# Performance work log

Measured on AMD Instinct MI355X. Metric: run time of the kernel, lower is better.

The kernel has to match this reference:

```python
import jax, jax.numpy as jnp
import numpy as np

N_STEPS = 5
N_ETYPES = 4
N_GRAPHS = 64
HEADS = 2
N, E, D = 50000, 600000, 128
C = 32


def setup_inputs() -> dict:
    key = jax.random.key(0)
    ks = jax.random.split(key, 24)
    s = 0.08  # param scale to keep activations well-conditioned
    return {
        "in_feat1": jax.random.normal(ks[0], (N, D), jnp.float32),
        "in_feat2": jax.random.normal(ks[1], (N, D), jnp.float32),
        "src1": jax.random.randint(ks[2], (E,), 0, N, jnp.int32),
        "dst1": jax.random.randint(ks[3], (E,), 0, N, jnp.int32),
        "etype1": jax.random.randint(ks[4], (E,), 0, N_ETYPES, jnp.int32),
        "gid1": jnp.sort(jax.random.randint(ks[5], (N,), 0, N_GRAPHS, jnp.int32)),
        "src2": jax.random.randint(ks[6], (E,), 0, N, jnp.int32),
        "dst2": jax.random.randint(ks[7], (E,), 0, N, jnp.int32),
        "etype2": jax.random.randint(ks[8], (E,), 0, N_ETYPES, jnp.int32),
        "gid2": jnp.sort(jax.random.randint(ks[9], (N,), 0, N_GRAPHS, jnp.int32)),
        "W_et": jax.random.normal(ks[10], (N_ETYPES, D, D), jnp.float32) * s,
        "b_et": jax.random.normal(ks[11], (N_ETYPES, D), jnp.float32) * s,
        "W_ih": jax.random.normal(ks[12], (3 * D, D), jnp.float32) * s,
        "W_hh": jax.random.normal(ks[13], (3 * D, D), jnp.float32) * s,
        "b_ih": jax.random.normal(ks[14], (3 * D,), jnp.float32) * s,
        "b_hh": jax.random.normal(ks[15], (3 * D,), jnp.float32) * s,
        "W_fc": jax.random.normal(ks[16], (HEADS * D, D), jnp.float32) * s,
        "attn_l": jax.random.normal(ks[17], (HEADS, D), jnp.float32) * s,
        "attn_r": jax.random.normal(ks[18], (HEADS, D), jnp.float32) * s,
        "gat_bias": jax.random.normal(ks[19], (HEADS * D,), jnp.float32) * s,
        "W_cls": jax.random.normal(ks[20], (C, D), jnp.float32) * s,
        "b_cls": jax.random.normal(ks[21], (C,), jnp.float32) * s,
    }


def _ggann(feat, src, dst, etype, gid,
           W_et, b_et, W_ih, W_hh, b_ih, b_hh,
           W_fc, attn_l, attn_r, gat_bias, W_cls, b_cls):
    n = feat.shape[0]
    h = feat  # in_feats == out_feats -> no zero-padding needed
    # ---- GatedGraphConv: n_steps of per-etype message passing + GRU ----
    for _ in range(N_STEPS):
        # per-etype linear on all nodes: [K, N, D]
        t = jnp.einsum('kod,nd->kno', W_et, h) + b_et[:, None, :]
        msg = t[etype, src]                         # [E, D] gather by (etype, src)
        a = jax.ops.segment_sum(msg, dst, num_segments=n)  # [N, D]
        # GRUCell(a, h)
        gi = a @ W_ih.T + b_ih                      # [N, 3D]
        gh = h @ W_hh.T + b_hh
        i_r, i_z, i_n = jnp.split(gi, 3, axis=1)
        h_r, h_z, h_n = jnp.split(gh, 3, axis=1)
        r = jax.nn.sigmoid(i_r + h_r)
        z = jax.nn.sigmoid(i_z + h_z)
        nn_ = jnp.tanh(i_n + r * h_n)
        h = (1.0 - z) * nn_ + z * h
    # F.normalize (L2 over dim=1) then sigmoid
    h = h / jnp.maximum(jnp.linalg.norm(h, axis=1, keepdims=True), 1e-12)
    h = jax.nn.sigmoid(h)
    # ---- GATConv (num_heads=2) ----
    zft = (h @ W_fc.T).reshape(n, HEADS, D)         # [N, H, D]
    el = jnp.sum(zft * attn_l[None], axis=-1)       # [N, H]
    er = jnp.sum(zft * attn_r[None], axis=-1)
    e = jax.nn.leaky_relu(el[src] + er[dst], 0.2)   # [E, H]
    m = jax.ops.segment_max(e, dst, num_segments=n)
    ex = jnp.exp(e - m[dst])
    den = jax.ops.segment_sum(ex, dst, num_segments=n)
    alpha = ex / den[dst]                           # edge softmax per dst, per head
    rst = jax.ops.segment_sum(alpha[:, :, None] * zft[src], dst, num_segments=n)
    rst = rst + gat_bias.reshape(1, HEADS, D)
    h = jax.nn.relu(rst)                            # [N, H, D] (dropout = eval identity)
    # ---- mean_nodes per graph + classify ----
    sums = jax.ops.segment_sum(h, gid, num_segments=N_GRAPHS)      # [B, H, D]
    cnt = jax.ops.segment_sum(jnp.ones((n, 1, 1), h.dtype), gid, num_segments=N_GRAPHS)
    hg = sums / jnp.maximum(cnt, 1.0)
    return hg @ W_cls.T + b_cls                     # [B, H, C]


def reference(in_feat1, in_feat2, src1, dst1, etype1, gid1,
              src2, dst2, etype2, gid2,
              W_et, b_et, W_ih, W_hh, b_ih, b_hh,
              W_fc, attn_l, attn_r, gat_bias, W_cls, b_cls):
    params = (W_et, b_et, W_ih, W_hh, b_ih, b_hh,
              W_fc, attn_l, attn_r, gat_bias, W_cls, b_cls)
    h1 = _ggann(in_feat1, src1, dst1, etype1, gid1, *params)  # [B, H, C]
    h2 = _ggann(in_feat2, src2, dst2, etype2, gid2, *params)
    # F.pairwise_distance(p=2, eps=1e-6) over last dim -> [B, H]
    dist = jnp.linalg.norm(h1 - h2 + 1e-6, axis=-1)
    return jax.nn.softmax(dist, axis=1)             # softmax over the 2 heads
```

## Files before the change

kernel.cpp:

```cpp
#include <hip/hip_runtime.h>
#include <math.h>

#define D 128
#define NG 64
#define NG2 128
#define NSTEPS 5

using short8 = __attribute__((ext_vector_type(8))) short;
using f32x4  = __attribute__((ext_vector_type(4))) float;
using f32x2  = __attribute__((ext_vector_type(2))) float;

__device__ __forceinline__ float sigf(float x) {
  float e = __expf(-fabsf(x));
  float inv = __fdividef(1.f, 1.f + e);
  return x >= 0.f ? inv : e * inv;
}
__device__ __forceinline__ float tanhf_fast(float x) {
  float e = __expf(-2.f * fabsf(x));
  float r = (1.f - e) * __fdividef(1.f, 1.f + e);
  return x >= 0.f ? r : -r;
}
__device__ __forceinline__ float lrelu(float x) { return x > 0.f ? x : 0.2f * x; }
__device__ __forceinline__ short f2bf(float x) {
  unsigned u = __float_as_uint(x);
  u += 0x7fff + ((u >> 16) & 1);
  return (short)(u >> 16);
}
__device__ __forceinline__ unsigned pk2(float x, float y) {
  return ((unsigned)(unsigned short)f2bf(y) << 16) | (unsigned short)f2bf(x);
}
__device__ __forceinline__ float bflo(unsigned v) { return __uint_as_float(v << 16); }
__device__ __forceinline__ float bfhi(unsigned v) { return __uint_as_float(v & 0xffff0000u); }
__device__ __forceinline__ float bf2f(short s) {
  return __uint_as_float(((unsigned)(unsigned short)s) << 16);
}
__device__ __forceinline__ unsigned char f2fp8(float x) {
  int p = __builtin_amdgcn_cvt_pk_fp8_f32(x, x, 0, false);
  return (unsigned char)(p & 0xff);
}

__device__ __forceinline__ void packK128(const float* __restrict__ W,
                                         short* __restrict__ P, int i) {
  int j = i & 7;
  int lane = (i >> 3) & 63;
  int kt = (i >> 9) & 3;
  int nt = i >> 11;
  int c = nt * 16 + (lane & 15);
  int k = kt * 32 + ((lane >> 4) << 3) + j;
  P[i] = f2bf(W[c * 128 + k]);
}
__device__ __forceinline__ void packA512f(const float* __restrict__ W_et,
                                          short* __restrict__ P, int i) {
  int j = i & 7;
  int lane = (i >> 3) & 63;
  int kt = (i >> 9) & 15;
  int nt = i >> 13;
  int c = nt * 16 + (lane & 15);
  int k = kt * 32 + ((lane >> 4) << 3) + j;
  P[i] = f2bf(W_et[(k >> 7) * 16384 + c * 128 + (k & 127)]);
}

__global__ __launch_bounds__(256) void k_setup(const float* __restrict__ W_et,
    const float* __restrict__ W_ih, const float* __restrict__ W_hh,
    const float* __restrict__ W_fc, const float* __restrict__ f1,
    const float* __restrict__ f2, short* __restrict__ WaP, short* __restrict__ WihP,
    short* __restrict__ WhhP, short* __restrict__ WfcP, short* __restrict__ hb,
    int* __restrict__ deg, int* __restrict__ gcnt, int N2, int Nd4) {
  const int sA = 65536, sB = 49152, sC = 49152, sD = 32768;
  int sE = N2, sF = NG2;
  long sG = 2L * Nd4;
  long tot = (long)(sA + sB + sC + sD) + sE + sF + sG;
  for (long ii = (long)blockIdx.x * blockDim.x + threadIdx.x; ii < tot;
       ii += (long)gridDim.x * blockDim.x) {
    long r = ii;
    if (r < sA) { packA512f(W_et, WaP, (int)r); continue; }
    r -= sA;
    if (r < sB) { packK128(W_ih, WihP, (int)r); continue; }
    r -= sB;
    if (r < sC) { packK128(W_hh, WhhP, (int)r); continue; }
    r -= sC;
    if (r < sD) { packK128(W_fc, WfcP, (int)r); continue; }
    r -= sD;
    if (r < sE) { deg[r] = 0; continue; }
    r -= sE;
    if (r < sF) { gcnt[r] = 0; continue; }
    r -= sF;
    {
      int i = (int)r;
      float4 v = (i < Nd4) ? ((const float4*)f1)[i] : ((const float4*)f2)[i - Nd4];
      ((uint2*)hb)[i] = make_uint2(pk2(v.x, v.y), pk2(v.z, v.w));
    }
  }
}

__global__ __launch_bounds__(256) void k_histgid(const int* __restrict__ dst1,
    const int* __restrict__ dst2, const int* __restrict__ gid1,
    const int* __restrict__ gid2, int E, int N, int* __restrict__ deg,
    int* __restrict__ gidc, int* __restrict__ gcnt, int EB) {
  __shared__ int cnt[NG2];
  if ((int)blockIdx.x < EB) {
    for (int e = blockIdx.x * 256 + threadIdx.x; e < 2 * E; e += EB * 256) {
      int d = (e < E) ? dst1[e] : dst2[e - E] + N;
      atomicAdd(&deg[d], 1);
    }
  } else {
    int t = threadIdx.x;
    if (t < NG2) cnt[t] = 0;
    __syncthreads();
    int i = (blockIdx.x - EB) * 256 + t;
    if (i < 2 * N) {
      int g = (i < N) ? gid1[i] : gid2[i - N] + NG;
      gidc[i] = g;
      atomicAdd(&cnt[g], 1);
    }
    __syncthreads();
    if (t < NG2 && cnt[t]) atomicAdd(&gcnt[t], cnt[t]);
  }
}

__global__ __launch_bounds__(256) void k_scan_a(const int* __restrict__ deg, int n,
                                                int* __restrict__ bsum) {
  int base = blockIdx.x * 1024 + threadIdx.x * 4;
  int s = 0;
  if (base + 3 < n) {
    int4 v = *(const int4*)(deg + base);
    s = v.x + v.y + v.z + v.w;
  } else {
    for (int k = 0; k < 4; ++k) if (base + k < n) s += deg[base + k];
  }
  #pragma unroll
  for (int off = 32; off; off >>= 1) s += __shfl_xor(s, off);
  __shared__ int ws[4];
  if ((threadIdx.x & 63) == 0) ws[threadIdx.x >> 6] = s;
  __syncthreads();
  if (threadIdx.x == 0) bsum[blockIdx.x] = ws[0] + ws[1] + ws[2] + ws[3];
}

__global__ __launch_bounds__(1024) void k_scan_b(const int* __restrict__ bsum,
                                                 int* __restrict__ boffs, int nb) {
  int tid = threadIdx.x;
  int v = (tid < nb) ? bsum[tid] : 0;
  int lane = tid & 63, wv = tid >> 6;
  int x = v;
  #pragma unroll
  for (int off = 1; off < 64; off <<= 1) {
    int y = __shfl_up(x, off);
    if (lane >= off) x += y;
  }
  __shared__ int wsum[16];
  if (lane == 63) wsum[wv] = x;
  __syncthreads();
  if (tid < 16) {
    int u = wsum[tid];
    #pragma unroll
    for (int off = 1; off < 16; off <<= 1) {
      int y = __shfl_up(u, off);
      if (tid >= off) u += y;
    }
    wsum[tid] = u;
  }
  __syncthreads();
  int woff = wv ? wsum[wv - 1] : 0;
  if (tid < nb) boffs[tid] = woff + x - v;
}

__global__ __launch_bounds__(256) void k_scan_c(const int* __restrict__ deg,
    const int* __restrict__ boffs, int* __restrict__ row_ofs,
    int* __restrict__ cursor, int n) {
  int base = blockIdx.x * 1024 + threadIdx.x * 4;
  int v[4] = {0, 0, 0, 0};
  if (base + 3 < n) {
    int4 t = *(const int4*)(deg + base);
    v[0] = t.x; v[1] = t.y; v[2] = t.z; v[3] = t.w;
  } else {
    for (int k = 0; k < 4; ++k) if (base + k < n) v[k] = deg[base + k];
  }
  int s = v[0] + v[1] + v[2] + v[3];
  int lane = threadIdx.x & 63, wv = threadIdx.x >> 6;
  int x = s;
  #pragma unroll
  for (int off = 1; off < 64; off <<= 1) {
    int y = __shfl_up(x, off);
    if (lane >= off) x += y;
  }
  __shared__ int wsum[4];
  if (lane == 63) wsum[wv] = x;
  __syncthreads();
  int woff = 0;
  for (int w = 0; w < wv; ++w) woff += wsum[w];
  int run = boffs[blockIdx.x] + woff + x - s;
  #pragma unroll
  for (int k = 0; k < 4; ++k) {
    int i = base + k;
    if (i < n) {
      cursor[i] = run;
      run += v[k];
      row_ofs[i + 1] = run;
    }
  }
  if (blockIdx.x == 0 && threadIdx.x == 0) row_ofs[0] = 0;
}

__global__ void k_scatter(const int* __restrict__ src1, const int* __restrict__ dst1,
                          const int* __restrict__ ety1, const int* __restrict__ src2,
                          const int* __restrict__ dst2, const int* __restrict__ ety2,
                          int E, int N, int* __restrict__ cursor,
                          int* __restrict__ csr_se) {
  for (int e = blockIdx.x * blockDim.x + threadIdx.x; e < 2 * E; e += gridDim.x * blockDim.x) {
    int s, d, et;
    if (e < E) { s = src1[e]; d = dst1[e]; et = ety1[e]; }
    else { s = src2[e - E] + N; d = dst2[e - E] + N; et = ety2[e - E]; }
    int p = atomicAdd(&cursor[d], 1);
    csr_se[p] = (s << 10) + et;
  }
}

__global__ __launch_bounds__(1024) void k_aggemm(const short* __restrict__ hb,
    const int* __restrict__ row_ofs, const int* __restrict__ csr_se,
    const short* __restrict__ WaP, const float* __restrict__ b_et,
    short* __restrict__ ab, int M) {
  __shared__ short Stile[16 * 512];
  __shared__ float lcnt[16][4];
  int tid = threadIdx.x;
  int lane = tid & 63, wave = tid >> 6;
  int row0 = blockIdx.x * 16;

  int li = wave;
  int node = row0 + li;
  f32x2 A0 = {0.f, 0.f}, A1 = {0.f, 0.f}, A2 = {0.f, 0.f}, A3 = {0.f, 0.f};
  int c0 = 0, c1 = 0, c2 = 0, c3 = 0;
  const char* hbb = (const char*)hb;
  if (node < M) {
    int beg = row_ofs[node], end = row_ofs[node + 1];
    #define ACC(ET, V) do { f32x2 t_; t_[0] = bflo(V); t_[1] = bfhi(V); \
        if (ET == 0)      { A0 += t_; ++c0; } \
        else if (ET == 1) { A1 += t_; ++c1; } \
        else if (ET == 2) { A2 += t_; ++c2; } \
        else              { A3 += t_; ++c3; } } while (0)
    for (int base = beg; base < end; base += 64) {
      int nv = end - base; if (nv > 64) nv = 64;
      int r = (lane < nv) ? csr_se[base + lane] : 0;
      int j = 0;
      for (; j + 16 <= nv; j += 16) {
        int rr[16];
        #pragma unroll
        for (int k = 0; k < 16; ++k) rr[k] = __builtin_amdgcn_readlane(r, j + k);
        unsigned v[16];
        #pragma unroll
        for (int k = 0; k < 16; ++k)
          v[k] = ((const unsigned*)(hbb + (rr[k] >> 2)))[lane];
        #pragma unroll
        for (int k = 0; k < 16; ++k) ACC(rr[k] & 3, v[k]);
      }
      for (; j + 8 <= nv; j += 8) {
        int rr[8];
        #pragma unroll
        for (int k = 0; k < 8; ++k) rr[k] = __builtin_amdgcn_readlane(r, j + k);
        unsigned v[8];
        #pragma unroll
        for (int k = 0; k < 8; ++k)
          v[k] = ((const unsigned*)(hbb + (rr[k] >> 2)))[lane];
        #pragma unroll
        for (int k = 0; k < 8; ++k) ACC(rr[k] & 3, v[k]);
      }
      for (; j + 4 <= nv; j += 4) {
        int rr[4];
        #pragma unroll
        for (int k = 0; k < 4; ++k) rr[k] = __builtin_amdgcn_readlane(r, j + k);
        unsigned v[4];
        #pragma unroll
        for (int k = 0; k < 4; ++k)
          v[k] = ((const unsigned*)(hbb + (rr[k] >> 2)))[lane];
        #pragma unroll
        for (int k = 0; k < 4; ++k) ACC(rr[k] & 3, v[k]);
      }
      for (; j < nv; ++j) {
        int rr = __builtin_amdgcn_readlane(r, j);
        unsigned v = ((const unsigned*)(hbb + (rr >> 2)))[lane];
        ACC(rr & 3, v);
      }
    }
    #undef ACC
  }
  {
    int swz = (li & 7) << 4;
    unsigned* ld = (unsigned*)Stile;
    ld[(li * 1024 + ((lane * 4      ) ^ swz)) >> 2] = pk2(A0[0], A0[1]);
    ld[(li * 1024 + ((lane * 4 + 256) ^ swz)) >> 2] = pk2(A1[0], A1[1]);
    ld[(li * 1024 + ((lane * 4 + 512) ^ swz)) >> 2] = pk2(A2[0], A2[1]);
    ld[(li * 1024 + ((lane * 4 + 768) ^ swz)) >> 2] = pk2(A3[0], A3[1]);
    if (lane == 0) {
      lcnt[li][0] = (float)c0; lcnt[li][1] = (float)c1;
      lcnt[li][2] = (float)c2; lcnt[li][3] = (float)c3;
    }
  }
  __syncthreads();

  if (wave < 8) {
    int quad = lane >> 4, l15 = lane & 15;
    int swz = (l15 & 7) << 4;
    int nt = wave;
    f32x4 acc = {0.f, 0.f, 0.f, 0.f};
    #pragma unroll
    for (int kt = 0; kt < 16; ++kt) {
      int boff = l15 * 1024 + ((kt * 64 + quad * 16) ^ swz);
      short8 a = *(const short8*)((const char*)Stile + boff);
      short8 b = *(const short8*)(WaP + (((size_t)(nt * 16 + kt) * 64) + lane) * 8);
      acc = __builtin_amdgcn_mfma_f32_16x16x32_bf16(a, b, acc, 0, 0, 0);
    }
    int c = nt * 16 + l15;
    float be0 = b_et[c], be1 = b_et[128 + c], be2 = b_et[256 + c], be3 = b_et[384 + c];
    #pragma unroll
    for (int reg = 0; reg < 4; ++reg) {
      int lr = quad * 4 + reg;
      int r = row0 + lr;
      if (r < M) {
        float v = acc[reg] + lcnt[lr][0] * be0 + lcnt[lr][1] * be1
                           + lcnt[lr][2] * be2 + lcnt[lr][3] * be3;
        ab[(size_t)r * 128 + c] = f2bf(v);
      }
    }
  }
}

__global__ __launch_bounds__(256) void k_gru_mfma(const short* __restrict__ ab,
    short* __restrict__ hb,
    const short* __restrict__ Pih, const short* __restrict__ Phh,
    const float* __restrict__ b_ih, const float* __restrict__ b_hh, int M) {
  int tid = threadIdx.x;
  int lane = tid & 63, wave = tid >> 6;
  int row0 = blockIdx.x * 128 + wave * 32;
  int quad = lane >> 4, l15 = lane & 15;
  short8 fa[2][4], fh[2][4];
  #pragma unroll
  for (int rt = 0; rt < 2; ++rt) {
    int ar = row0 + rt * 16 + l15; if (ar >= M) ar = M - 1;
    #pragma unroll
    for (int kt = 0; kt < 4; ++kt) {
      fa[rt][kt] = *(const short8*)(ab + (size_t)ar * 128 + kt * 32 + quad * 8);
      fh[rt][kt] = *(const short8*)(hb + (size_t)ar * 128 + kt * 32 + quad * 8);
    }
  }
  for (int nt = 0; nt < 8; ++nt) {
    f32x4 accr[2], accz[2], acci[2], acch[2];
    #pragma unroll
    for (int rt = 0; rt < 2; ++rt) {
      accr[rt] = {0.f,0.f,0.f,0.f}; accz[rt] = {0.f,0.f,0.f,0.f};
      acci[rt] = {0.f,0.f,0.f,0.f}; acch[rt] = {0.f,0.f,0.f,0.f};
    }
    #pragma unroll
    for (int kt = 0; kt < 4; ++kt) {
      size_t li = ((size_t)lane) * 8;
      short8 wr = *(const short8*)(Pih + ((size_t)((nt     ) * 4 + kt) * 64) * 8 + li);
      short8 wz = *(const short8*)(Pih + ((size_t)((nt +  8) * 4 + kt) * 64) * 8 + li);
      short8 wn = *(const short8*)(Pih + ((size_t)((nt + 16) * 4 + kt) * 64) * 8 + li);
      short8 ur = *(const short8*)(Phh + ((size_t)((nt     ) * 4 + kt) * 64) * 8 + li);
      short8 uz = *(const short8*)(Phh + ((size_t)((nt +  8) * 4 + kt) * 64) * 8 + li);
      short8 un = *(const short8*)(Phh + ((size_t)((nt + 16) * 4 + kt) * 64) * 8 + li);
      #pragma unroll
      for (int rt = 0; rt < 2; ++rt) {
        accr[rt] = __builtin_amdgcn_mfma_f32_16x16x32_bf16(fa[rt][kt], wr, accr[rt], 0, 0, 0);
        accr[rt] = __builtin_amdgcn_mfma_f32_16x16x32_bf16(fh[rt][kt], ur, accr[rt], 0, 0, 0);
        accz[rt] = __builtin_amdgcn_mfma_f32_16x16x32_bf16(fa[rt][kt], wz, accz[rt], 0, 0, 0);
        accz[rt] = __builtin_amdgcn_mfma_f32_16x16x32_bf16(fh[rt][kt], uz, accz[rt], 0, 0, 0);
        acci[rt] = __builtin_amdgcn_mfma_f32_16x16x32_bf16(fa[rt][kt], wn, acci[rt], 0, 0, 0);
        acch[rt] = __builtin_amdgcn_mfma_f32_16x16x32_bf16(fh[rt][kt], un, acch[rt], 0, 0, 0);
      }
    }
    int c = nt * 16 + l15;
    float bir = b_ih[c],      bhr = b_hh[c];
    float biz = b_ih[c+128],  bhz = b_hh[c+128];
    float bin_= b_ih[c+256],  bhn = b_hh[c+256];
    #pragma unroll
    for (int rt = 0; rt < 2; ++rt) {
      #pragma unroll
      for (int reg = 0; reg < 4; ++reg) {
        int r = row0 + rt * 16 + quad * 4 + reg;
        if (r < M) {
          float rg = sigf(accr[rt][reg] + bir + bhr);
          float zg = sigf(accz[rt][reg] + biz + bhz);
          float ng = tanhf_fast(acci[rt][reg] + bin_ + rg * (acch[rt][reg] + bhn));
          float hold = bf2f(hb[(size_t)r * 128 + c]);
          float hn2 = (1.f - zg) * ng + zg * hold;
          hb[(size_t)r * 128 + c] = f2bf(hn2);
        }
      }
    }
  }
}

__global__ __launch_bounds__(256) void k_fc_eler(const short* __restrict__ Ab,
    const short* __restrict__ Bp, const float* __restrict__ attn_l,
    const float* __restrict__ attn_r, unsigned char* __restrict__ zq,
    float* __restrict__ el, float* __restrict__ er, int M) {
  int tid = threadIdx.x;
  int lane = tid & 63, wave = tid >> 6;
  int row0 = blockIdx.x * 128 + wave * 32;
  int quad = lane >> 4, l15 = lane & 15;
  short8 af[2][4];
  #pragma unroll
  for (int rt = 0; rt < 2; ++rt) {
    int ar = row0 + rt * 16 + l15; if (ar >= M) ar = M - 1;
    #pragma unroll
    for (int kt = 0; kt < 4; ++kt)
      af[rt][kt] = *(const short8*)(Ab + (size_t)ar * 128 + kt * 32 + quad * 8);
  }
  #pragma unroll
  for (int rt = 0; rt < 2; ++rt) {
    float ss = 0.f;
    #pragma unroll
    for (int kt = 0; kt < 4; ++kt)
      #pragma unroll
      for (int j = 0; j < 8; ++j) {
        float x = bf2f(af[rt][kt][j]);
        ss += x * x;
      }
    ss += __shfl_xor(ss, 16);
    ss += __shfl_xor(ss, 32);
    float inv = 1.f / fmaxf(sqrtf(ss), 1e-12f);
    #pragma unroll
    for (int kt = 0; kt < 4; ++kt)
      #pragma unroll
      for (int j = 0; j < 8; ++j)
        af[rt][kt][j] = f2bf(sigf(bf2f(af[rt][kt][j]) * inv));
  }
  float elp[2][2][4] = {};
  float erp[2][2][4] = {};
  for (int nt = 0; nt < 16; ++nt) {
    f32x4 a0 = {0.f,0.f,0.f,0.f}, a1 = {0.f,0.f,0.f,0.f};
    #pragma unroll
    for (int kt = 0; kt < 4; ++kt) {
      short8 b = *(const short8*)(Bp + (((size_t)(nt * 4 + kt) * 64) + lane) * 8);
      a0 = __builtin_amdgcn_mfma_f32_16x16x32_bf16(af[0][kt], b, a0, 0, 0, 0);
      a1 = __builtin_amdgcn_mfma_f32_16x16x32_bf16(af[1][kt], b, a1, 0, 0, 0);
    }
    int head = nt >> 3;
    int colh = (nt & 7) * 16 + l15;
    float alv = attn_l[head * 128 + colh];
    float arv = attn_r[head * 128 + colh];
    int c = nt * 16 + l15;
    #pragma unroll
    for (int rt = 0; rt < 2; ++rt) {
      f32x4 acc = rt ? a1 : a0;
      #pragma unroll
      for (int reg = 0; reg < 4; ++reg) {
        int r = row0 + rt * 16 + quad * 4 + reg;
        if (r < M) zq[(size_t)r * 256 + c] = f2fp8(acc[reg]);
        elp[rt][head][reg] += acc[reg] * alv;
        erp[rt][head][reg] += acc[reg] * arv;
      }
    }
  }
  #pragma unroll
  for (int off = 1; off < 16; off <<= 1) {
    #pragma unroll
    for (int rt = 0; rt < 2; ++rt)
      #pragma unroll
      for (int h = 0; h < 2; ++h)
        #pragma unroll
        for (int reg = 0; reg < 4; ++reg) {
          elp[rt][h][reg] += __shfl_xor(elp[rt][h][reg], off);
          erp[rt][h][reg] += __shfl_xor(erp[rt][h][reg], off);
        }
  }
  if (l15 == 0) {
    #pragma unroll
    for (int rt = 0; rt < 2; ++rt)
      #pragma unroll
      for (int h = 0; h < 2; ++h)
        #pragma unroll
        for (int reg = 0; reg < 4; ++reg) {
          int r = row0 + rt * 16 + quad * 4 + reg;
          if (r < M) {
            el[r * 2 + h] = elp[rt][h][reg];
            er[r * 2 + h] = erp[rt][h][reg];
          }
        }
  }
}

__global__ __launch_bounds__(256) void k_gat(const unsigned char* __restrict__ zq,
    const float* __restrict__ el, const float* __restrict__ er,
    const int* __restrict__ row_ofs, const int* __restrict__ csr_se,
    const float* __restrict__ gat_bias, short* __restrict__ outb,
    float* __restrict__ sums, int N) {
  if (blockIdx.x < NG2) sums[blockIdx.x * 256 + threadIdx.x] = 0.f;
  int node = blockIdx.x * 4 + (threadIdx.x >> 6);
  int lane = threadIdx.x & 63;
  if (node >= N) return;
  int beg = row_ofs[node], end = row_ofs[node + 1];
  float2 ern = ((const float2*)er)[node];
  float l0 = 0.f, l1 = 0.f;
  float4 acc = {0.f, 0.f, 0.f, 0.f};
  int head = lane >> 5;
  const char* elb = (const char*)el;
  const char* zqb = (const char*)zq;
  for (int base = beg; base < end; base += 64) {
    int nv = end - base; if (nv > 64) nv = 64;
    int se = (lane < nv) ? csr_se[base + lane] : 0;
    float p0 = 0.f, p1 = 0.f;
    if (lane < nv) {
      float2 els = *(const float2*)(elb + (se >> 7));
      p0 = expf(lrelu(els.x + ern.x));
      p1 = expf(lrelu(els.y + ern.y));
    }
    float t0 = p0, t1 = p1;
    #pragma unroll
    for (int off = 32; off; off >>= 1) { t0 += __shfl_xor(t0, off); t1 += __shfl_xor(t1, off); }
    l0 += t0; l1 += t1;
    int w01 = (int)pk2(p0, p1);
    int j = 0;
    for (; j + 8 <= nv; j += 8) {
      int bb[8]; unsigned ww[8];
      #pragma unroll
      for (int k = 0; k < 8; ++k) {
        bb[k] = __builtin_amdgcn_readlane(se, j + k) >> 2;
        ww[k] = (unsigned)__builtin_amdgcn_readlane(w01, j + k);
      }
      unsigned zz[8];
      #pragma unroll
      for (int k = 0; k < 8; ++k)
        zz[k] = ((const unsigned*)(zqb + bb[k]))[lane];
      #pragma unroll
      for (int k = 0; k < 8; ++k) {
        float f = head ? bfhi(ww[k]) : bflo(ww[k]);
        f32x2 lo = __builtin_amdgcn_cvt_pk_f32_fp8(zz[k], false);
        f32x2 hi = __builtin_amdgcn_cvt_pk_f32_fp8(zz[k], true);
        acc.x += f * lo[0]; acc.y += f * lo[1];
        acc.z += f * hi[0]; acc.w += f * hi[1];
      }
    }
    for (; j + 4 <= nv; j += 4) {
      int bb[4]; unsigned ww[4];
      #pragma unroll
      for (int k = 0; k < 4; ++k) {
        bb[k] = __builtin_amdgcn_readlane(se, j + k) >> 2;
        ww[k] = (unsigned)__builtin_amdgcn_readlane(w01, j + k);
      }
      unsigned zz[4];
      #pragma unroll
      for (int k = 0; k < 4; ++k)
        zz[k] = ((const unsigned*)(zqb + bb[k]))[lane];
      #pragma unroll
      for (int k = 0; k < 4; ++k) {
        float f = head ? bfhi(ww[k]) : bflo(ww[k]);
        f32x2 lo = __builtin_amdgcn_cvt_pk_f32_fp8(zz[k], false);
        f32x2 hi = __builtin_amdgcn_cvt_pk_f32_fp8(zz[k], true);
        acc.x += f * lo[0]; acc.y += f * lo[1];
        acc.z += f * hi[0]; acc.w += f * hi[1];
      }
    }
    for (; j < nv; ++j) {
      int bj = __builtin_amdgcn_readlane(se, j) >> 2;
      unsigned wj = (unsigned)__builtin_amdgcn_readlane(w01, j);
      float w = head ? bfhi(wj) : bflo(wj);
      unsigned zv = ((const unsigned*)(zqb + bj))[lane];
      f32x2 lo = __builtin_amdgcn_cvt_pk_f32_fp8(zv, false);
      f32x2 hi = __builtin_amdgcn_cvt_pk_f32_fp8(zv, true);
      acc.x += w * lo[0]; acc.y += w * lo[1];
      acc.z += w * hi[0]; acc.w += w * hi[1];
    }
  }
  float inv0 = (l0 > 0.f) ? 1.f / l0 : 0.f;
  float inv1 = (l1 > 0.f) ? 1.f / l1 : 0.f;
  float inv = head ? inv1 : inv0;
  float4 b = ((const float4*)gat_bias)[lane];
  float ox = fmaxf(acc.x * inv + b.x, 0.f);
  float oy = fmaxf(acc.y * inv + b.y, 0.f);
  float oz = fmaxf(acc.z * inv + b.z, 0.f);
  float ow = fmaxf(acc.w * inv + b.w, 0.f);
  ((uint2*)(outb + (size_t)node * 256))[lane] = make_uint2(pk2(ox, oy), pk2(oz, ow));
}

__global__ __launch_bounds__(256) void k_segred(const short* __restrict__ hgatb,
    const int* __restrict__ gidc, float* __restrict__ sums, int NT2) {
  int node0 = blockIdx.x * 128;
  int col = threadIdx.x;
  int end = node0 + 128; if (end > NT2) end = NT2;
  if (node0 >= NT2) return;
  float acc = 0.f;
  int gcur = gidc[node0];
  for (int n = node0; n < end; ++n) {
    int g = gidc[n];
    if (g != gcur) {
      atomicAdd(&sums[gcur * 256 + col], acc);
      acc = 0.f; gcur = g;
    }
    acc += bf2f(hgatb[(size_t)n * 256 + col]);
  }
  atomicAdd(&sums[gcur * 256 + col], acc);
}

__global__ __launch_bounds__(64) void k_classify(const float* __restrict__ sums,
    const int* __restrict__ gcnt, const float* __restrict__ W_cls,
    const float* __restrict__ b_cls, float* __restrict__ logits) {
  int g = blockIdx.x, tid = threadIdx.x;
  int hh = tid >> 5, c = tid & 31;
  float invc = 1.f / fmaxf((float)gcnt[g], 1.f);
  float acc = 0.f;
  for (int d = 0; d < D; ++d)
    acc += (sums[g * 256 + hh * D + d] * invc) * W_cls[c * D + d];
  logits[g * 64 + hh * 32 + c] = acc + b_cls[c];
}

__global__ __launch_bounds__(64) void k_final(const float* __restrict__ logits,
    float* __restrict__ out) {
  int g = threadIdx.x;
  if (g >= NG) return;
  float d[2];
  #pragma unroll
  for (int hh = 0; hh < 2; ++hh) {
    float s = 0.f;
    for (int c = 0; c < 32; ++c) {
      float df = logits[g * 64 + hh * 32 + c] - logits[(g + NG) * 64 + hh * 32 + c] + 1e-6f;
      s += df * df;
    }
    d[hh] = sqrtf(s);
  }
  float mx = fmaxf(d[0], d[1]);
  float e0 = expf(d[0] - mx), e1 = expf(d[1] - mx);
  float den = e0 + e1;
  out[g * 2] = e0 / den;
  out[g * 2 + 1] = e1 / den;
}

extern "C" void kernel_launch(void* const* d_in, const int* in_sizes, int n_in,
                              void* d_out, int out_size, void* d_ws, size_t ws_size,
                              hipStream_t stream) {
  const float* in_feat1 = (const float*)d_in[0];
  const float* in_feat2 = (const float*)d_in[1];
  const int* src1 = (const int*)d_in[2];
  const int* dst1 = (const int*)d_in[3];
  const int* ety1 = (const int*)d_in[4];
  const int* gid1 = (const int*)d_in[5];
  const int* src2 = (const int*)d_in[6];
  const int* dst2 = (const int*)d_in[7];
  const int* ety2 = (const int*)d_in[8];
  const int* gid2 = (const int*)d_in[9];
  const float* W_et = (const float*)d_in[10];
  const float* b_et = (const float*)d_in[11];
  const float* W_ih = (const float*)d_in[12];
  const float* W_hh = (const float*)d_in[13];
  const float* b_ih = (const float*)d_in[14];
  const float* b_hh = (const float*)d_in[15];
  const float* W_fc = (const float*)d_in[16];
  const float* attn_l = (const float*)d_in[17];
  const float* attn_r = (const float*)d_in[18];
  const float* gat_bias = (const float*)d_in[19];
  const float* W_cls = (const float*)d_in[20];
  const float* b_cls = (const float*)d_in[21];
  float* out = (float*)d_out;

  int N = in_sizes[0] / D;
  int E = in_sizes[2];
  int N2 = 2 * N, E2 = 2 * E;

  char* p = (char*)d_ws;
  auto alloc = [&](size_t bytes) -> void* {
    char* r = p;
    p += (bytes + 255) & ~(size_t)255;
    return (void*)r;
  };
  short* WaP  = (short*)alloc((size_t)512 * 128 * 2);
  short* WihP = (short*)alloc((size_t)384 * 128 * 2);
  short* WhhP = (short*)alloc((size_t)384 * 128 * 2);
  short* WfcP = (short*)alloc((size_t)256 * 128 * 2);
  short* hb  = (short*)alloc((size_t)N2 * D * 2);
  short* ab  = (short*)alloc((size_t)N2 * D * 2);
  short* hgatb = (short*)alloc((size_t)N2 * 256 * 2);
  unsigned char* zq = (unsigned char*)alloc((size_t)N2 * 256);
  float* el  = (float*)alloc((size_t)N2 * 2 * 4);
  float* er  = (float*)alloc((size_t)N2 * 2 * 4);
  float* sums= (float*)alloc((size_t)NG2 * 256 * 4);
  float* logits = (float*)alloc((size_t)NG2 * 64 * 4);
  int* deg     = (int*)alloc((size_t)N2 * 4);
  int* row_ofs = (int*)alloc(((size_t)N2 + 1) * 4);
  int* cursor  = (int*)alloc((size_t)N2 * 4);
  int* gidc    = (int*)alloc((size_t)N2 * 4);
  int* gcnt    = (int*)alloc((size_t)NG2 * 4);
  int* bsum    = (int*)alloc((size_t)1024 * 4);
  int* boffs   = (int*)alloc((size_t)1024 * 4);
  int* csr_se  = (int*)alloc((size_t)E2 * 4);
  if ((size_t)(p - (char*)d_ws) > ws_size) return;

  k_setup<<<dim3(2048), dim3(256), 0, stream>>>(W_et, W_ih, W_hh, W_fc,
      in_feat1, in_feat2, WaP, WihP, WhhP, WfcP, hb, deg, gcnt, N2, N * D / 4);

  int EB = (E2 + 255) / 256;
  int GB = (N2 + 255) / 256;
  int nb = (N2 + 1023) / 1024;
  k_histgid<<<dim3(EB + GB), dim3(256), 0, stream>>>(dst1, dst2, gid1, gid2,
                                                     E, N, deg, gidc, gcnt, EB);
  k_scan_a<<<dim3(nb), dim3(256), 0, stream>>>(deg, N2, bsum);
  k_scan_b<<<dim3(1), dim3(1024), 0, stream>>>(bsum, boffs, nb);
  k_scan_c<<<dim3(nb), dim3(256), 0, stream>>>(deg, boffs, row_ofs, cursor, N2);
  k_scatter<<<dim3(EB), dim3(256), 0, stream>>>(src1, dst1, ety1, src2, dst2, ety2,
                                                E, N, cursor, csr_se);

  int gb16 = (N2 + 15) / 16;
  int gb128 = (N2 + 127) / 128;
  int nb4 = (N2 + 3) / 4;

  for (int s = 0; s < NSTEPS; ++s) {
    k_aggemm<<<dim3(gb16), dim3(1024), 0, stream>>>(hb, row_ofs, csr_se, WaP, b_et, ab, N2);
    k_gru_mfma<<<dim3(gb128), dim3(256), 0, stream>>>(ab, hb, WihP, WhhP, b_ih, b_hh, N2);
  }
  k_fc_eler<<<dim3(gb128), dim3(256), 0, stream>>>(hb, WfcP, attn_l, attn_r, zq, el, er, N2);
  k_gat<<<dim3(nb4), dim3(256), 0, stream>>>(zq, el, er, row_ofs, csr_se,
                                             gat_bias, hgatb, sums, N2);
  k_segred<<<dim3((N2 + 127) / 128), dim3(256), 0, stream>>>(hgatb, gidc, sums, N2);
  k_classify<<<dim3(NG2), dim3(64), 0, stream>>>(sums, gcnt, W_cls, b_cls, logits);
  k_final<<<dim3(1), dim3(64), 0, stream>>>(logits, out);
}
```

Before: 1.185 ms.

## Gather neighbor features in FP8 and slice CSR build atomics by destination range

Keeps an FP8 copy of the hidden state, written at setup and in the GRU epilogue, and has the per-step neighbor aggregation gather 2-byte FP8 pairs instead of 4-byte bf16 pairs. This halves the random-gather traffic in the dominant aggregation loop, at the cost of reduced precision in the aggregated messages. The degree histogram and the CSR scatter are also split into 8 destination slices, each block handling one slice, so atomics land in a narrower address range. The trade-off is that every edge index gets read 8 times.

```diff
diff --git a/kernel.cpp b/kernel.cpp
--- a/kernel.cpp
+++ b/kernel.cpp
@@ -65,6 +65,7 @@
     const float* __restrict__ W_fc, const float* __restrict__ f1,
     const float* __restrict__ f2, short* __restrict__ WaP, short* __restrict__ WihP,
     short* __restrict__ WhhP, short* __restrict__ WfcP, short* __restrict__ hb,
+    unsigned char* __restrict__ hq,
     int* __restrict__ deg, int* __restrict__ gcnt, int N2, int Nd4) {
   const int sA = 65536, sB = 49152, sC = 49152, sD = 32768;
   int sE = N2, sF = NG2;
@@ -89,6 +90,9 @@
       int i = (int)r;
       float4 v = (i < Nd4) ? ((const float4*)f1)[i] : ((const float4*)f2)[i - Nd4];
       ((uint2*)hb)[i] = make_uint2(pk2(v.x, v.y), pk2(v.z, v.w));
+      int q = __builtin_amdgcn_cvt_pk_fp8_f32(v.x, v.y, 0, false);
+      q = __builtin_amdgcn_cvt_pk_fp8_f32(v.z, v.w, q, true);
+      ((unsigned*)hq)[i] = (unsigned)q;
     }
   }
 }
@@ -96,12 +100,17 @@
 __global__ __launch_bounds__(256) void k_histgid(const int* __restrict__ dst1,
     const int* __restrict__ dst2, const int* __restrict__ gid1,
     const int* __restrict__ gid2, int E, int N, int* __restrict__ deg,
-    int* __restrict__ gidc, int* __restrict__ gcnt, int EB) {
+    int* __restrict__ gidc, int* __restrict__ gcnt, int EB, int N2) {
   __shared__ int cnt[NG2];
   if ((int)blockIdx.x < EB) {
-    for (int e = blockIdx.x * 256 + threadIdx.x; e < 2 * E; e += EB * 256) {
+    int slice = blockIdx.x & 7;
+    int bls = blockIdx.x >> 3;
+    int nbs = EB >> 3;
+    int W = (N2 + 7) >> 3;
+    int lo = slice * W, hi = lo + W;
+    for (int e = bls * 256 + threadIdx.x; e < 2 * E; e += nbs * 256) {
       int d = (e < E) ? dst1[e] : dst2[e - E] + N;
-      atomicAdd(&deg[d], 1);
+      if (d >= lo && d < hi) atomicAdd(&deg[d], 1);
     }
   } else {
     int t = threadIdx.x;
@@ -201,21 +210,28 @@
   if (blockIdx.x == 0 && threadIdx.x == 0) row_ofs[0] = 0;
 }
 
-__global__ void k_scatter(const int* __restrict__ src1, const int* __restrict__ dst1,
-                          const int* __restrict__ ety1, const int* __restrict__ src2,
-                          const int* __restrict__ dst2, const int* __restrict__ ety2,
-                          int E, int N, int* __restrict__ cursor,
-                          int* __restrict__ csr_se) {
-  for (int e = blockIdx.x * blockDim.x + threadIdx.x; e < 2 * E; e += gridDim.x * blockDim.x) {
-    int s, d, et;
-    if (e < E) { s = src1[e]; d = dst1[e]; et = ety1[e]; }
-    else { s = src2[e - E] + N; d = dst2[e - E] + N; et = ety2[e - E]; }
+__global__ __launch_bounds__(256) void k_scatter(const int* __restrict__ src1,
+    const int* __restrict__ dst1, const int* __restrict__ ety1,
+    const int* __restrict__ src2, const int* __restrict__ dst2,
+    const int* __restrict__ ety2, int E, int N, int* __restrict__ cursor,
+    int* __restrict__ csr_se, int N2) {
+  int slice = blockIdx.x & 7;
+  int bls = blockIdx.x >> 3;
+  int nbs = gridDim.x >> 3;
+  int W = (N2 + 7) >> 3;
+  int lo = slice * W, hi = lo + W;
+  for (int e = bls * 256 + threadIdx.x; e < 2 * E; e += nbs * 256) {
+    int d = (e < E) ? dst1[e] : dst2[e - E] + N;
+    if (d < lo || d >= hi) continue;
+    int s, et;
+    if (e < E) { s = src1[e]; et = ety1[e]; }
+    else { s = src2[e - E] + N; et = ety2[e - E]; }
     int p = atomicAdd(&cursor[d], 1);
     csr_se[p] = (s << 10) + et;
   }
 }
 
-__global__ __launch_bounds__(1024) void k_aggemm(const short* __restrict__ hb,
+__global__ __launch_bounds__(1024) void k_aggemm(const unsigned char* __restrict__ hq,
     const int* __restrict__ row_ofs, const int* __restrict__ csr_se,
     const short* __restrict__ WaP, const float* __restrict__ b_et,
     short* __restrict__ ab, int M) {
@@ -229,10 +245,11 @@
   int node = row0 + li;
   f32x2 A0 = {0.f, 0.f}, A1 = {0.f, 0.f}, A2 = {0.f, 0.f}, A3 = {0.f, 0.f};
   int c0 = 0, c1 = 0, c2 = 0, c3 = 0;
-  const char* hbb = (const char*)hb;
+  const char* hqb = (const char*)hq;
   if (node < M) {
     int beg = row_ofs[node], end = row_ofs[node + 1];
-    #define ACC(ET, V) do { f32x2 t_; t_[0] = bflo(V); t_[1] = bfhi(V); \
+    #define ACC(ET, V) do { \
+        f32x2 t_ = __builtin_amdgcn_cvt_pk_f32_fp8((unsigned)(V), false); \
         if (ET == 0)      { A0 += t_; ++c0; } \
         else if (ET == 1) { A1 += t_; ++c1; } \
         else if (ET == 2) { A2 += t_; ++c2; } \
@@ -245,10 +262,10 @@
         int rr[16];
         #pragma unroll
         for (int k = 0; k < 16; ++k) rr[k] = __builtin_amdgcn_readlane(r, j + k);
-        unsigned v[16];
+        unsigned short v[16];
         #pragma unroll
         for (int k = 0; k < 16; ++k)
-          v[k] = ((const unsigned*)(hbb + (rr[k] >> 2)))[lane];
+          v[k] = ((const unsigned short*)(hqb + (rr[k] >> 3)))[lane];
         #pragma unroll
         for (int k = 0; k < 16; ++k) ACC(rr[k] & 3, v[k]);
       }
@@ -256,10 +273,10 @@
         int rr[8];
         #pragma unroll
         for (int k = 0; k < 8; ++k) rr[k] = __builtin_amdgcn_readlane(r, j + k);
-        unsigned v[8];
+        unsigned short v[8];
         #pragma unroll
         for (int k = 0; k < 8; ++k)
-          v[k] = ((const unsigned*)(hbb + (rr[k] >> 2)))[lane];
+          v[k] = ((const unsigned short*)(hqb + (rr[k] >> 3)))[lane];
         #pragma unroll
         for (int k = 0; k < 8; ++k) ACC(rr[k] & 3, v[k]);
       }
@@ -267,16 +284,16 @@
         int rr[4];
         #pragma unroll
         for (int k = 0; k < 4; ++k) rr[k] = __builtin_amdgcn_readlane(r, j + k);
-        unsigned v[4];
+        unsigned short v[4];
         #pragma unroll
         for (int k = 0; k < 4; ++k)
-          v[k] = ((const unsigned*)(hbb + (rr[k] >> 2)))[lane];
+          v[k] = ((const unsigned short*)(hqb + (rr[k] >> 3)))[lane];
         #pragma unroll
         for (int k = 0; k < 4; ++k) ACC(rr[k] & 3, v[k]);
       }
       for (; j < nv; ++j) {
         int rr = __builtin_amdgcn_readlane(r, j);
-        unsigned v = ((const unsigned*)(hbb + (rr >> 2)))[lane];
+        unsigned short v = ((const unsigned short*)(hqb + (rr >> 3)))[lane];
         ACC(rr & 3, v);
       }
     }
@@ -324,7 +341,7 @@
 }
 
 __global__ __launch_bounds__(256) void k_gru_mfma(const short* __restrict__ ab,
-    short* __restrict__ hb,
+    short* __restrict__ hb, unsigned char* __restrict__ hq,
     const short* __restrict__ Pih, const short* __restrict__ Phh,
     const float* __restrict__ b_ih, const float* __restrict__ b_hh, int M) {
   int tid = threadIdx.x;
@@ -383,6 +400,7 @@
           float hold = bf2f(hb[(size_t)r * 128 + c]);
           float hn2 = (1.f - zg) * ng + zg * hold;
           hb[(size_t)r * 128 + c] = f2bf(hn2);
+          hq[(size_t)r * 128 + c] = f2fp8(hn2);
         }
       }
     }
@@ -666,6 +684,7 @@
   short* WhhP = (short*)alloc((size_t)384 * 128 * 2);
   short* WfcP = (short*)alloc((size_t)256 * 128 * 2);
   short* hb  = (short*)alloc((size_t)N2 * D * 2);
+  unsigned char* hq = (unsigned char*)alloc((size_t)N2 * D);
   short* ab  = (short*)alloc((size_t)N2 * D * 2);
   short* hgatb = (short*)alloc((size_t)N2 * 256 * 2);
   unsigned char* zq = (unsigned char*)alloc((size_t)N2 * 256);
@@ -684,26 +703,26 @@
   if ((size_t)(p - (char*)d_ws) > ws_size) return;
 
   k_setup<<<dim3(2048), dim3(256), 0, stream>>>(W_et, W_ih, W_hh, W_fc,
-      in_feat1, in_feat2, WaP, WihP, WhhP, WfcP, hb, deg, gcnt, N2, N * D / 4);
-
-  int EB = (E2 + 255) / 256;
+      in_feat1, in_feat2, WaP, WihP, WhhP, WfcP, hb, hq, deg, gcnt, N2, N * D / 4);
+
+  int EB = 4800;
   int GB = (N2 + 255) / 256;
   int nb = (N2 + 1023) / 1024;
   k_histgid<<<dim3(EB + GB), dim3(256), 0, stream>>>(dst1, dst2, gid1, gid2,
-                                                     E, N, deg, gidc, gcnt, EB);
+                                                     E, N, deg, gidc, gcnt, EB, N2);
   k_scan_a<<<dim3(nb), dim3(256), 0, stream>>>(deg, N2, bsum);
   k_scan_b<<<dim3(1), dim3(1024), 0, stream>>>(bsum, boffs, nb);
   k_scan_c<<<dim3(nb), dim3(256), 0, stream>>>(deg, boffs, row_ofs, cursor, N2);
-  k_scatter<<<dim3(EB), dim3(256), 0, stream>>>(src1, dst1, ety1, src2, dst2, ety2,
-                                                E, N, cursor, csr_se);
+  k_scatter<<<dim3(4800), dim3(256), 0, stream>>>(src1, dst1, ety1, src2, dst2, ety2,
+                                                  E, N, cursor, csr_se, N2);
 
   int gb16 = (N2 + 15) / 16;
   int gb128 = (N2 + 127) / 128;
   int nb4 = (N2 + 3) / 4;
 
   for (int s = 0; s < NSTEPS; ++s) {
-    k_aggemm<<<dim3(gb16), dim3(1024), 0, stream>>>(hb, row_ofs, csr_se, WaP, b_et, ab, N2);
-    k_gru_mfma<<<dim3(gb128), dim3(256), 0, stream>>>(ab, hb, WihP, WhhP, b_ih, b_hh, N2);
+    k_aggemm<<<dim3(gb16), dim3(1024), 0, stream>>>(hq, row_ofs, csr_se, WaP, b_et, ab, N2);
+    k_gru_mfma<<<dim3(gb128), dim3(256), 0, stream>>>(ab, hb, hq, WihP, WhhP, b_ih, b_hh, N2);
   }
   k_fc_eler<<<dim3(gb128), dim3(256), 0, stream>>>(hb, WfcP, attn_l, attn_r, zq, el, er, N2);
   k_gat<<<dim3(nb4), dim3(256), 0, stream>>>(zq, el, er, row_ofs, csr_se,
```

Measured after the change: 1.197 ms. Within noise of the previous version (+1.0%).
